# Optimization experiments

Hardware: AMD Instinct MI355X
Metric: run time of the kernel (lower is better)

Reference implementation:

```python
import jax, jax.numpy as jnp
import numpy as np

B, S, D = 1, 4096, 2048
H = 16
HD = D // H  # 128
BASE = 10000.0


def setup_inputs() -> dict:
    key = jax.random.key(0)
    ks = jax.random.split(key, 6)
    hidden_states = jax.random.normal(ks[0], (B, S, D), dtype=jnp.float32)
    position_ids = jnp.broadcast_to(jnp.arange(S, dtype=jnp.int64 if jax.config.jax_enable_x64 else jnp.int32), (B, S))
    scale = 1.0 / np.sqrt(D)
    Wq = jax.random.normal(ks[1], (D, D), dtype=jnp.float32) * scale
    Wk = jax.random.normal(ks[2], (D, D), dtype=jnp.float32) * scale
    Wv = jax.random.normal(ks[3], (D, D), dtype=jnp.float32) * scale
    Wo = jax.random.normal(ks[4], (D, D), dtype=jnp.float32) * scale
    return {"hidden_states": hidden_states, "Wq": Wq, "Wk": Wk, "Wv": Wv, "Wo": Wo, "position_ids": position_ids}


def _rotate_half(x):
    x1, x2 = x[..., : x.shape[-1] // 2], x[..., x.shape[-1] // 2 :]
    return jnp.concatenate((-x2, x1), axis=-1)


def reference(hidden_states, Wq, Wk, Wv, Wo, position_ids):
    # QKV projections (torch Linear: x @ W.T)
    q = hidden_states @ Wq.T  # [B,S,D]
    k = hidden_states @ Wk.T
    v = hidden_states @ Wv.T
    # split heads -> [B,H,S,HD]
    q = q.reshape(B, S, H, HD).transpose(0, 2, 1, 3)
    k = k.reshape(B, S, H, HD).transpose(0, 2, 1, 3)
    v = v.reshape(B, S, H, HD).transpose(0, 2, 1, 3)
    # RoPE tables over seq positions
    inv_freq = 1.0 / (BASE ** (jnp.arange(0, HD, 2, dtype=jnp.float32) / HD))  # [HD/2]
    t = jnp.arange(S, dtype=jnp.float32)
    freqs = t[:, None] * inv_freq[None, :]            # [S, HD/2]
    emb = jnp.concatenate((freqs, freqs), axis=-1)    # [S, HD]
    cos = jnp.cos(emb)[position_ids][:, None]         # [B,1,S,HD]
    sin = jnp.sin(emb)[position_ids][:, None]
    q = q * cos + _rotate_half(q) * sin
    k = k * cos + _rotate_half(k) * sin
    # attention (num_kv_heads == num_heads, so no GQA repeat)
    scores = jnp.einsum("bhqd,bhkd->bhqk", q, k) / jnp.sqrt(jnp.float32(HD))
    attn = jax.nn.softmax(scores, axis=-1)
    out = jnp.einsum("bhqk,bhkd->bhqd", attn, v)      # [B,H,S,HD]
    out = out.transpose(0, 2, 1, 3).reshape(B, S, D)
    return out @ Wo.T
```

## Files before the change

### kernel.cpp

```cpp
#include <hip/hip_runtime.h>
#include <hip/hip_bf16.h>

#define S_LEN 4096
#define DMODEL 2048
#define NHEADS 16
#define HEADDIM 128
#define LDQ 6144

typedef __attribute__((ext_vector_type(8))) short bf16x8;
typedef __attribute__((ext_vector_type(4))) float f32x4;

__device__ __forceinline__ float bf2f(ushort u) {
  union { unsigned int i; float f; } x; x.i = ((unsigned int)u) << 16; return x.f;
}
__device__ __forceinline__ ushort f2bf(float f) {
  union { float f; unsigned int i; } x; x.f = f;
  unsigned int u = x.i;
  unsigned int r = u + 0x7fffu + ((u >> 16) & 1u);
  return (ushort)(r >> 16);
}
__device__ __forceinline__ unsigned int cvtpk(float a, float b) {
  unsigned int r;
  asm("v_cvt_pk_bf16_f32 %0, %1, %2" : "=v"(r) : "v"(a), "v"(b));
  return r;
}
__device__ __forceinline__ float fexp2(float x) {
  float r;
  asm("v_exp_f32 %0, %1" : "=v"(r) : "v"(x));
  return r;
}

__device__ __forceinline__ void gload16(const ushort* g, ushort* l) {
  __builtin_amdgcn_global_load_lds(
      (const __attribute__((address_space(1))) unsigned int*)g,
      (__attribute__((address_space(3))) unsigned int*)l, 16, 0, 0);
}

__global__ __launch_bounds__(256) void rope_table_kernel(float* __restrict__ cosT,
                                                         float* __restrict__ sinT) {
  int idx = blockIdx.x * 256 + threadIdx.x;
  int t = idx >> 6, j = idx & 63;
  float expo = (float)(2 * j) / 128.0f;
  float inv = 1.0f / powf(10000.0f, expo);
  float f = (float)t * inv;
  cosT[idx] = cosf(f);
  sinT[idx] = sinf(f);
}

__global__ __launch_bounds__(256) void convert_kernel(const float* __restrict__ in,
                                                      ushort* __restrict__ hi) {
  int i = (blockIdx.x * 256 + threadIdx.x) * 4;
  float4 v = *reinterpret_cast<const float4*>(&in[i]);
  ushort4 h;
  h.x = f2bf(v.x); h.y = f2bf(v.y); h.z = f2bf(v.z); h.w = f2bf(v.w);
  *reinterpret_cast<ushort4*>(&hi[i]) = h;
}

__global__ __launch_bounds__(256) void prep_weights(const float* __restrict__ Wq,
                                                    const float* __restrict__ Wk,
                                                    const float* __restrict__ Wv,
                                                    const float* __restrict__ Wo,
                                                    ushort* __restrict__ Wqkv,
                                                    ushort* __restrict__ Woh) {
  int i = (blockIdx.x * 256 + threadIdx.x) * 4;
  int which = blockIdx.y;
  const float* src = (which == 0) ? Wq : (which == 1) ? Wk : (which == 2) ? Wv : Wo;
  ushort* dst = (which == 3) ? Woh : (Wqkv + (size_t)which * DMODEL * DMODEL);
  float4 v = *reinterpret_cast<const float4*>(&src[i]);
  ushort4 h;
  h.x = f2bf(v.x); h.y = f2bf(v.y); h.z = f2bf(v.z); h.w = f2bf(v.w);
  *reinterpret_cast<ushort4*>(&dst[i]) = h;
}

__global__ __launch_bounds__(256) void gemm_qkv(const ushort* __restrict__ Ah_,
                                                const ushort* __restrict__ Bh_,
                                                ushort* __restrict__ Cout,
                                                int M, int N, int K) {
  __shared__ __align__(16) ushort sAh[128 * 64], sBh[128 * 64];
  const int tid = threadIdx.x;
  const int wave = tid >> 6, lane = tid & 63;
  const int lg = lane >> 4, lm = lane & 15;
  const int nwg = gridDim.x * gridDim.y;
  const int id = blockIdx.y * gridDim.x + blockIdx.x;
  const int cpx = nwg >> 3;
  const int swz = (id & 7) * cpx + (id >> 3);
  const int nbx = N >> 7;
  const int m0 = (swz / nbx) * 128, n0 = (swz % nbx) * 128;
  const int wm = (wave >> 1) * 64, wn = (wave & 1) * 64;
  f32x4 acc[4][4] = {};

  int srow[4], scc[4], lbs[4];
#pragma unroll
  for (int it = 0; it < 4; ++it) {
    int ci = it * 256 + wave * 64 + lane;
    srow[it] = ci >> 3;
    scc[it] = (ci & 7) ^ (srow[it] & 7);
    lbs[it] = (it * 256 + wave * 64) * 8;
  }

  for (int k0 = 0; k0 < K; k0 += 64) {
    __syncthreads();
#pragma unroll
    for (int it = 0; it < 4; ++it) {
      size_t ga = (size_t)(m0 + srow[it]) * K + k0 + scc[it] * 8;
      size_t gb = (size_t)(n0 + srow[it]) * K + k0 + scc[it] * 8;
      gload16(&Ah_[ga], &sAh[lbs[it]]);
      gload16(&Bh_[gb], &sBh[lbs[it]]);
    }
    __syncthreads();
    bf16x8 ah[4][2], bh[4][2];
#pragma unroll
    for (int t = 0; t < 4; ++t)
#pragma unroll
      for (int kc = 0; kc < 2; ++kc) {
        int Ra = wm + t * 16 + lm;
        int Rb = wn + t * 16 + lm;
        int pa_ = ((kc * 4 + lg) ^ (Ra & 7)) * 8;
        int pb_ = ((kc * 4 + lg) ^ (Rb & 7)) * 8;
        ah[t][kc] = *reinterpret_cast<const bf16x8*>(&sAh[Ra * 64 + pa_]);
        bh[t][kc] = *reinterpret_cast<const bf16x8*>(&sBh[Rb * 64 + pb_]);
      }
#pragma unroll
    for (int kc = 0; kc < 2; ++kc)
#pragma unroll
      for (int mi = 0; mi < 4; ++mi)
#pragma unroll
        for (int ni = 0; ni < 4; ++ni)
          acc[mi][ni] = __builtin_amdgcn_mfma_f32_16x16x32_bf16(ah[mi][kc], bh[ni][kc], acc[mi][ni], 0, 0, 0);
  }
#pragma unroll
  for (int mi = 0; mi < 4; ++mi)
#pragma unroll
    for (int ni = 0; ni < 4; ++ni)
#pragma unroll
      for (int j = 0; j < 4; ++j) {
        int row = m0 + wm + mi * 16 + lg * 4 + j;
        int col = n0 + wn + ni * 16 + lm;
        Cout[(size_t)row * N + col] = f2bf(acc[mi][ni][j]);
      }
}

__global__ __launch_bounds__(256) void gemm1o64(const ushort* __restrict__ Ah_,
                                                const ushort* __restrict__ Bh_,
                                                float* __restrict__ Cout,
                                                int M, int N, int K) {
  __shared__ __align__(16) ushort sAh[128 * 64], sBh[128 * 64];
  const int tid = threadIdx.x;
  const int wave = tid >> 6, lane = tid & 63;
  const int lg = lane >> 4, lm = lane & 15;
  const int nwg = gridDim.x * gridDim.y;
  const int id = blockIdx.y * gridDim.x + blockIdx.x;
  const int cpx = nwg >> 3;
  const int swz = (id & 7) * cpx + (id >> 3);
  const int nbx = N >> 7;
  const int m0 = (swz / nbx) * 128, n0 = (swz % nbx) * 128;
  const int wm = (wave >> 1) * 64, wn = (wave & 1) * 64;
  f32x4 acc[4][4] = {};

  int srow[4], scc[4], lbs[4];
#pragma unroll
  for (int it = 0; it < 4; ++it) {
    int ci = it * 256 + wave * 64 + lane;
    srow[it] = ci >> 3;
    scc[it] = (ci & 7) ^ (srow[it] & 7);
    lbs[it] = (it * 256 + wave * 64) * 8;
  }

  for (int k0 = 0; k0 < K; k0 += 64) {
    __syncthreads();
#pragma unroll
    for (int it = 0; it < 4; ++it) {
      size_t ga = (size_t)(m0 + srow[it]) * K + k0 + scc[it] * 8;
      size_t gb = (size_t)(n0 + srow[it]) * K + k0 + scc[it] * 8;
      gload16(&Ah_[ga], &sAh[lbs[it]]);
      gload16(&Bh_[gb], &sBh[lbs[it]]);
    }
    __syncthreads();
    bf16x8 ah[4][2], bh[4][2];
#pragma unroll
    for (int t = 0; t < 4; ++t)
#pragma unroll
      for (int kc = 0; kc < 2; ++kc) {
        int Ra = wm + t * 16 + lm;
        int Rb = wn + t * 16 + lm;
        int pa_ = ((kc * 4 + lg) ^ (Ra & 7)) * 8;
        int pb_ = ((kc * 4 + lg) ^ (Rb & 7)) * 8;
        ah[t][kc] = *reinterpret_cast<const bf16x8*>(&sAh[Ra * 64 + pa_]);
        bh[t][kc] = *reinterpret_cast<const bf16x8*>(&sBh[Rb * 64 + pb_]);
      }
#pragma unroll
    for (int kc = 0; kc < 2; ++kc)
#pragma unroll
      for (int mi = 0; mi < 4; ++mi)
#pragma unroll
        for (int ni = 0; ni < 4; ++ni)
          acc[mi][ni] = __builtin_amdgcn_mfma_f32_16x16x32_bf16(ah[mi][kc], bh[ni][kc], acc[mi][ni], 0, 0, 0);
  }
#pragma unroll
  for (int mi = 0; mi < 4; ++mi)
#pragma unroll
    for (int ni = 0; ni < 4; ++ni)
#pragma unroll
      for (int j = 0; j < 4; ++j) {
        int row = m0 + wm + mi * 16 + lg * 4 + j;
        int col = n0 + wn + ni * 16 + lm;
        Cout[(size_t)row * N + col] = acc[mi][ni][j];
      }
}

__global__ __launch_bounds__(256) void rope2_kernel(ushort* __restrict__ QKV,
                                                    const int* __restrict__ pos,
                                                    const float* __restrict__ cosT,
                                                    const float* __restrict__ sinT) {
  int t = blockIdx.x * 256 + threadIdx.x;
  int j0 = (t & 7) * 8;
  int hh = (t >> 3) & 15;
  int s = t >> 7;
  int p = pos[s];
  float cs[8], sn[8];
  *reinterpret_cast<float4*>(&cs[0]) = *reinterpret_cast<const float4*>(&cosT[p * 64 + j0]);
  *reinterpret_cast<float4*>(&cs[4]) = *reinterpret_cast<const float4*>(&cosT[p * 64 + j0 + 4]);
  *reinterpret_cast<float4*>(&sn[0]) = *reinterpret_cast<const float4*>(&sinT[p * 64 + j0]);
  *reinterpret_cast<float4*>(&sn[4]) = *reinterpret_cast<const float4*>(&sinT[p * 64 + j0 + 4]);
  size_t base = (size_t)s * LDQ + hh * HEADDIM + j0;
  union u8 { uint4 v; ushort e[8]; };
  u8 qa, qb, ka, kb;
  qa.v = *reinterpret_cast<const uint4*>(&QKV[base]);
  qb.v = *reinterpret_cast<const uint4*>(&QKV[base + 64]);
  ka.v = *reinterpret_cast<const uint4*>(&QKV[base + DMODEL]);
  kb.v = *reinterpret_cast<const uint4*>(&QKV[base + DMODEL + 64]);
  const float scl = 0.12751742f;
#pragma unroll
  for (int e = 0; e < 8; ++e) {
    float q1 = bf2f(qa.e[e]), q2 = bf2f(qb.e[e]);
    float k1 = bf2f(ka.e[e]), k2 = bf2f(kb.e[e]);
    qa.e[e] = f2bf((q1 * cs[e] - q2 * sn[e]) * scl);
    qb.e[e] = f2bf((q2 * cs[e] + q1 * sn[e]) * scl);
    ka.e[e] = f2bf(k1 * cs[e] - k2 * sn[e]);
    kb.e[e] = f2bf(k2 * cs[e] + k1 * sn[e]);
  }
  *reinterpret_cast<uint4*>(&QKV[base]) = qa.v;
  *reinterpret_cast<uint4*>(&QKV[base + 64]) = qb.v;
  *reinterpret_cast<uint4*>(&QKV[base + DMODEL]) = ka.v;
  *reinterpret_cast<uint4*>(&QKV[base + DMODEL + 64]) = kb.v;
}

__global__ __launch_bounds__(256) void transpose_kernel(const ushort* __restrict__ Vr,
                                                        ushort* __restrict__ Vt) {
  __shared__ __align__(16) ushort tile[64 * 72];
  int tid = threadIdx.x;
  int s0 = blockIdx.x * 64, c0 = blockIdx.y * 64;
#pragma unroll
  for (int it = 0; it < 2; ++it) {
    int i = tid + it * 256;
    int r = i >> 3, c = i & 7;
    *reinterpret_cast<uint4*>(&tile[r * 72 + c * 8]) =
        *reinterpret_cast<const uint4*>(&Vr[(size_t)(s0 + r) * LDQ + c0 + c * 8]);
  }
  __syncthreads();
#pragma unroll
  for (int it = 0; it < 2; ++it) {
    int i = tid + it * 256;
    int cr = i >> 3, sc = i & 7;
    ushort tmp[8];
#pragma unroll
    for (int j = 0; j < 8; ++j) tmp[j] = tile[(sc * 8 + j) * 72 + cr];
    *reinterpret_cast<uint4*>(&Vt[(size_t)(c0 + cr) * S_LEN + s0 + sc * 8]) =
        *reinterpret_cast<uint4*>(tmp);
  }
}

__global__ __launch_bounds__(256, 2) void flash12_kernel(const ushort* __restrict__ QKV,
                                                         const ushort* __restrict__ Vt,
                                                         ushort* __restrict__ Oh) {
  __shared__ __align__(16) ushort Kt[2][64 * 128];
  __shared__ __align__(16) ushort Vs[2][128 * 64];
  const int tid = threadIdx.x;
  const int wave = tid >> 6, lane = tid & 63;
  const int lg = lane >> 4, lm = lane & 15;
  const int id = blockIdx.y * gridDim.x + blockIdx.x;
  const int o = (id & 7) * 64 + (id >> 3);
  const int h = o >> 5;
  const int q0 = (o & 31) * 128;

  bf16x8 qh[2][4];
#pragma unroll
  for (int t2 = 0; t2 < 2; ++t2) {
    int qrow = q0 + wave * 32 + t2 * 16 + lm;
#pragma unroll
    for (int kc = 0; kc < 4; ++kc)
      qh[t2][kc] = *reinterpret_cast<const bf16x8*>(
          &QKV[(size_t)qrow * LDQ + h * HEADDIM + kc * 32 + lg * 8]);
  }

  bf16x8 ones;
#pragma unroll
  for (int i = 0; i < 8; ++i) ones[i] = (short)0x3f80;

  auto rho = [](int s) {
    return 32 * ((s >> 4) & 1) + 8 * ((s >> 2) & 3) + 4 * (s >> 5) + (s & 3);
  };
  const ushort* Kb = QKV + DMODEL;
  const ushort* pK[4];
  const ushort* pV[4];
  int lbs[4];
#pragma unroll
  for (int k = 0; k < 4; ++k) {
    int ci = k * 256 + wave * 64 + lane;
    int ks = ci >> 4;
    int kcc = (ci & 15) ^ (ks & 7);
    pK[k] = Kb + (size_t)rho(ks) * LDQ + h * HEADDIM + kcc * 8;
    int vd = ci >> 3;
    int vcc = (ci & 7) ^ (vd & 7);
    pV[k] = Vt + (size_t)(h * HEADDIM + vd) * S_LEN + vcc * 8;
    lbs[k] = (k * 256 + wave * 64) * 8;
  }

  f32x4 oacc[2][8] = {};
  f32x4 osum[2] = {};
  float mrun[2];
#pragma unroll
  for (int t2 = 0; t2 < 2; ++t2) mrun[t2] = -3.0e38f;

#pragma unroll
  for (int k = 0; k < 4; ++k) {
    gload16(pK[k], &Kt[0][lbs[k]]);
    gload16(pV[k], &Vs[0][lbs[k]]);
  }
  __syncthreads();

  for (int t = 0; t < S_LEN / 64; ++t) {
    const int cur = t & 1;
    if (t < S_LEN / 64 - 1) {
      const size_t koff = (size_t)(t + 1) * 64;
#pragma unroll
      for (int k = 0; k < 4; ++k) {
        gload16(pK[k] + koff * LDQ, &Kt[cur ^ 1][lbs[k]]);
        gload16(pV[k] + koff, &Vs[cur ^ 1][lbs[k]]);
      }
    }
    const ushort* Kc = &Kt[cur][0];
    const ushort* Vc = &Vs[cur][0];

    f32x4 st[2][4] = {};
    __builtin_amdgcn_s_setprio(1);
#pragma unroll
    for (int nf = 0; nf < 4; ++nf)
#pragma unroll
      for (int kc = 0; kc < 4; ++kc) {
        int pc = (kc * 4 + lg) ^ (lm & 7);
        bf16x8 kfrag = *reinterpret_cast<const bf16x8*>(&Kc[(nf * 16 + lm) * 128 + pc * 8]);
        st[0][nf] = __builtin_amdgcn_mfma_f32_16x16x32_bf16(kfrag, qh[0][kc], st[0][nf], 0, 0, 0);
        st[1][nf] = __builtin_amdgcn_mfma_f32_16x16x32_bf16(kfrag, qh[1][kc], st[1][nf], 0, 0, 0);
      }
    __builtin_amdgcn_s_setprio(0);

    float m16[2];
#pragma unroll
    for (int t2 = 0; t2 < 2; ++t2) {
      float m = fmaxf(st[t2][0][0], st[t2][0][1]);
      m = fmaxf(fmaxf(m, st[t2][0][2]), st[t2][0][3]);
      m = fmaxf(fmaxf(m, st[t2][1][0]), st[t2][1][1]);
      m = fmaxf(fmaxf(m, st[t2][1][2]), st[t2][1][3]);
      m = fmaxf(fmaxf(m, st[t2][2][0]), st[t2][2][1]);
      m = fmaxf(fmaxf(m, st[t2][2][2]), st[t2][2][3]);
      m = fmaxf(fmaxf(m, st[t2][3][0]), st[t2][3][1]);
      m = fmaxf(fmaxf(m, st[t2][3][2]), st[t2][3][3]);
      m = fmaxf(m, __shfl_xor(m, 16));
      m = fmaxf(m, __shfl_xor(m, 32));
      m16[t2] = m;
    }

    bool grow = (m16[0] > mrun[0] + 11.5f) || (m16[1] > mrun[1] + 11.5f);
    if (__any(grow)) {
#pragma unroll
      for (int t2 = 0; t2 < 2; ++t2) {
        float mn = fmaxf(mrun[t2], m16[t2]);
        float scl = fexp2(mrun[t2] - mn);
        mrun[t2] = mn;
        float sj[4];
#pragma unroll
        for (int j = 0; j < 4; ++j) sj[j] = __shfl(scl, lg * 4 + j);
#pragma unroll
        for (int j = 0; j < 4; ++j) osum[t2][j] *= sj[j];
#pragma unroll
        for (int nb = 0; nb < 8; ++nb)
#pragma unroll
          for (int j = 0; j < 4; ++j) oacc[t2][nb][j] *= sj[j];
      }
    }

#pragma unroll
    for (int t2 = 0; t2 < 2; ++t2)
#pragma unroll
      for (int nf = 0; nf < 4; ++nf)
#pragma unroll
        for (int j = 0; j < 4; ++j)
          st[t2][nf][j] = fexp2(st[t2][nf][j] - mrun[t2]);

    bf16x8 pa[2][2];
#pragma unroll
    for (int t2 = 0; t2 < 2; ++t2)
#pragma unroll
      for (int kk = 0; kk < 2; ++kk) {
        union { unsigned int u[4]; bf16x8 v; } w_;
        w_.u[0] = cvtpk(st[t2][kk][0], st[t2][kk][1]);
        w_.u[1] = cvtpk(st[t2][kk][2], st[t2][kk][3]);
        w_.u[2] = cvtpk(st[t2][2 + kk][0], st[t2][2 + kk][1]);
        w_.u[3] = cvtpk(st[t2][2 + kk][2], st[t2][2 + kk][3]);
        pa[t2][kk] = w_.v;
      }

    __builtin_amdgcn_s_setprio(1);
#pragma unroll
    for (int t2 = 0; t2 < 2; ++t2) {
      osum[t2] = __builtin_amdgcn_mfma_f32_16x16x32_bf16(pa[t2][0], ones, osum[t2], 0, 0, 0);
      osum[t2] = __builtin_amdgcn_mfma_f32_16x16x32_bf16(pa[t2][1], ones, osum[t2], 0, 0, 0);
    }
#pragma unroll
    for (int nb = 0; nb < 8; ++nb)
#pragma unroll
      for (int kk = 0; kk < 2; ++kk) {
        int pc = (kk * 4 + lg) ^ (lm & 7);
        bf16x8 vfrag = *reinterpret_cast<const bf16x8*>(&Vc[(nb * 16 + lm) * 64 + pc * 8]);
        oacc[0][nb] = __builtin_amdgcn_mfma_f32_16x16x32_bf16(pa[0][kk], vfrag, oacc[0][nb], 0, 0, 0);
        oacc[1][nb] = __builtin_amdgcn_mfma_f32_16x16x32_bf16(pa[1][kk], vfrag, oacc[1][nb], 0, 0, 0);
      }
    __builtin_amdgcn_s_setprio(0);

    __syncthreads();
  }

#pragma unroll
  for (int t2 = 0; t2 < 2; ++t2) {
    float linv[4];
#pragma unroll
    for (int j = 0; j < 4; ++j) linv[j] = 1.0f / osum[t2][j];
#pragma unroll
    for (int nb = 0; nb < 8; ++nb)
#pragma unroll
      for (int j = 0; j < 4; ++j) {
        int row = q0 + wave * 32 + t2 * 16 + lg * 4 + j;
        int col = h * HEADDIM + nb * 16 + lm;
        Oh[(size_t)row * DMODEL + col] = f2bf(oacc[t2][nb][j] * linv[j]);
      }
  }
}

extern "C" void kernel_launch(void* const* d_in, const int* in_sizes, int n_in,
                              void* d_out, int out_size, void* d_ws, size_t ws_size,
                              hipStream_t stream) {
  (void)in_sizes; (void)n_in; (void)out_size; (void)ws_size;
  const float* X  = (const float*)d_in[0];
  const float* Wq = (const float*)d_in[1];
  const float* Wk = (const float*)d_in[2];
  const float* Wv = (const float*)d_in[3];
  const float* Wo = (const float*)d_in[4];
  const int* pos  = (const int*)d_in[5];
  float* out = (float*)d_out;

  ushort* wb = (ushort*)d_ws;
  const size_t SD = (size_t)S_LEN * DMODEL;
  const size_t DD = (size_t)DMODEL * DMODEL;

  ushort* Xh   = wb;
  ushort* QKV  = wb + 2 * SD;
  ushort* Vt   = wb + 5 * SD;
  ushort* W0h  = wb + 6 * SD;
  ushort* Wqkv = wb + 7 * SD;
  float* cosT  = (float*)(wb + 9 * SD);
  float* sinT  = cosT + (size_t)S_LEN * 64;
  ushort* OhB  = Wqkv;

  rope_table_kernel<<<S_LEN * 64 / 256, 256, 0, stream>>>(cosT, sinT);
  convert_kernel<<<SD / 1024, 256, 0, stream>>>(X, Xh);
  prep_weights<<<dim3(DD / 1024, 4), 256, 0, stream>>>(Wq, Wk, Wv, Wo, Wqkv, W0h);

  gemm_qkv<<<dim3(LDQ / 128, S_LEN / 128), 256, 0, stream>>>(Xh, Wqkv, QKV, S_LEN, LDQ, DMODEL);

  rope2_kernel<<<(S_LEN * 1024 / 8) / 256, 256, 0, stream>>>(QKV, pos, cosT, sinT);
  transpose_kernel<<<dim3(S_LEN / 64, DMODEL / 64), 256, 0, stream>>>(QKV + 2 * DMODEL, Vt);

  flash12_kernel<<<dim3(32, 16), 256, 0, stream>>>(QKV, Vt, OhB);

  dim3 gemmGrid(DMODEL / 128, S_LEN / 128);
  gemm1o64<<<gemmGrid, 256, 0, stream>>>(OhB, W0h, out, S_LEN, DMODEL, DMODEL);
}
```

Measured before the change: 340.5 us.

## Software-pipeline flash attention by computing next tile's QK^T before the barrier

Restructures the attention main loop into a manually unrolled pair of tile steps with named LDS buffers and two score register sets. After the PV product and the barrier for tile T, the kernel issues the global loads for tile T+2 and immediately computes QK^T for tile T+1. The aim is to let the next tile's score matrix multiplies overlap with the softmax and exponent work instead of serialising them. The cost is a second score accumulator array, which raises register pressure under the 2-blocks-per-CU launch bound and may cause spills.

```diff
diff --git a/kernel.cpp b/kernel.cpp
--- a/kernel.cpp
+++ b/kernel.cpp
@@ -270,11 +270,92 @@
   }
 }
 
-__global__ __launch_bounds__(256, 2) void flash12_kernel(const ushort* __restrict__ QKV,
+#define FTILE(STC, STN, VCUR, KWB, VWB, KRB, T)                                           \
+  {                                                                                       \
+    float m16[2];                                                                         \
+    _Pragma("unroll") for (int t2 = 0; t2 < 2; ++t2) {                                    \
+      float m = fmaxf(STC[t2][0][0], STC[t2][0][1]);                                      \
+      m = fmaxf(fmaxf(m, STC[t2][0][2]), STC[t2][0][3]);                                  \
+      m = fmaxf(fmaxf(m, STC[t2][1][0]), STC[t2][1][1]);                                  \
+      m = fmaxf(fmaxf(m, STC[t2][1][2]), STC[t2][1][3]);                                  \
+      m = fmaxf(fmaxf(m, STC[t2][2][0]), STC[t2][2][1]);                                  \
+      m = fmaxf(fmaxf(m, STC[t2][2][2]), STC[t2][2][3]);                                  \
+      m = fmaxf(fmaxf(m, STC[t2][3][0]), STC[t2][3][1]);                                  \
+      m = fmaxf(fmaxf(m, STC[t2][3][2]), STC[t2][3][3]);                                  \
+      m = fmaxf(m, __shfl_xor(m, 16));                                                    \
+      m = fmaxf(m, __shfl_xor(m, 32));                                                    \
+      m16[t2] = m;                                                                        \
+    }                                                                                     \
+    bool grow = (m16[0] > mrun[0] + 11.5f) || (m16[1] > mrun[1] + 11.5f);                 \
+    if (__any(grow)) {                                                                    \
+      _Pragma("unroll") for (int t2 = 0; t2 < 2; ++t2) {                                  \
+        float mn = fmaxf(mrun[t2], m16[t2]);                                              \
+        float scl = fexp2(mrun[t2] - mn);                                                 \
+        mrun[t2] = mn;                                                                    \
+        float sj[4];                                                                      \
+        _Pragma("unroll") for (int j = 0; j < 4; ++j) sj[j] = __shfl(scl, lg * 4 + j);    \
+        _Pragma("unroll") for (int j = 0; j < 4; ++j) osum[t2][j] *= sj[j];               \
+        _Pragma("unroll") for (int nb = 0; nb < 8; ++nb)                                  \
+            _Pragma("unroll") for (int j = 0; j < 4; ++j) oacc[t2][nb][j] *= sj[j];       \
+      }                                                                                   \
+    }                                                                                     \
+    _Pragma("unroll") for (int t2 = 0; t2 < 2; ++t2)                                      \
+        _Pragma("unroll") for (int nf = 0; nf < 4; ++nf)                                  \
+            _Pragma("unroll") for (int j = 0; j < 4; ++j)                                 \
+                STC[t2][nf][j] = fexp2(STC[t2][nf][j] - mrun[t2]);                        \
+    bf16x8 pa[2][2];                                                                      \
+    _Pragma("unroll") for (int t2 = 0; t2 < 2; ++t2)                                      \
+        _Pragma("unroll") for (int kk = 0; kk < 2; ++kk) {                                \
+      union { unsigned int u[4]; bf16x8 v; } w_;                                          \
+      w_.u[0] = cvtpk(STC[t2][kk][0], STC[t2][kk][1]);                                    \
+      w_.u[1] = cvtpk(STC[t2][kk][2], STC[t2][kk][3]);                                    \
+      w_.u[2] = cvtpk(STC[t2][2 + kk][0], STC[t2][2 + kk][1]);                            \
+      w_.u[3] = cvtpk(STC[t2][2 + kk][2], STC[t2][2 + kk][3]);                            \
+      pa[t2][kk] = w_.v;                                                                  \
+    }                                                                                     \
+    __builtin_amdgcn_s_setprio(1);                                                        \
+    _Pragma("unroll") for (int t2 = 0; t2 < 2; ++t2) {                                    \
+      osum[t2] = __builtin_amdgcn_mfma_f32_16x16x32_bf16(pa[t2][0], ones, osum[t2], 0, 0, 0); \
+      osum[t2] = __builtin_amdgcn_mfma_f32_16x16x32_bf16(pa[t2][1], ones, osum[t2], 0, 0, 0); \
+    }                                                                                     \
+    _Pragma("unroll") for (int nb = 0; nb < 8; ++nb)                                      \
+        _Pragma("unroll") for (int kk = 0; kk < 2; ++kk) {                                \
+      int pc = (kk * 4 + lg) ^ (lm & 7);                                                  \
+      bf16x8 vfrag = *reinterpret_cast<const bf16x8*>(&VCUR[(nb * 16 + lm) * 64 + pc * 8]); \
+      oacc[0][nb] = __builtin_amdgcn_mfma_f32_16x16x32_bf16(pa[0][kk], vfrag, oacc[0][nb], 0, 0, 0); \
+      oacc[1][nb] = __builtin_amdgcn_mfma_f32_16x16x32_bf16(pa[1][kk], vfrag, oacc[1][nb], 0, 0, 0); \
+    }                                                                                     \
+    __builtin_amdgcn_s_setprio(0);                                                        \
+    __syncthreads();                                                                      \
+    if ((T) + 2 < 64) {                                                                   \
+      const size_t ko_ = (size_t)((T) + 2) * 64;                                          \
+      _Pragma("unroll") for (int k = 0; k < 4; ++k) {                                     \
+        gload16(pK[k] + ko_ * LDQ, &KWB[lbs[k]]);                                         \
+        gload16(pV[k] + ko_, &VWB[lbs[k]]);                                               \
+      }                                                                                   \
+    }                                                                                     \
+    if ((T) + 1 < 64) {                                                                   \
+      _Pragma("unroll") for (int t2 = 0; t2 < 2; ++t2)                                    \
+          _Pragma("unroll") for (int nf = 0; nf < 4; ++nf) STN[t2][nf] = fzero;           \
+      __builtin_amdgcn_s_setprio(1);                                                      \
+      _Pragma("unroll") for (int nf = 0; nf < 4; ++nf)                                    \
+          _Pragma("unroll") for (int kc = 0; kc < 4; ++kc) {                              \
+        int pc = (kc * 4 + lg) ^ (lm & 7);                                                \
+        bf16x8 kfrag = *reinterpret_cast<const bf16x8*>(&KRB[(nf * 16 + lm) * 128 + pc * 8]); \
+        STN[0][nf] = __builtin_amdgcn_mfma_f32_16x16x32_bf16(kfrag, qh[0][kc], STN[0][nf], 0, 0, 0); \
+        STN[1][nf] = __builtin_amdgcn_mfma_f32_16x16x32_bf16(kfrag, qh[1][kc], STN[1][nf], 0, 0, 0); \
+      }                                                                                   \
+      __builtin_amdgcn_s_setprio(0);                                                      \
+    }                                                                                     \
+  }
+
+__global__ __launch_bounds__(256, 2) void flash14_kernel(const ushort* __restrict__ QKV,
                                                          const ushort* __restrict__ Vt,
                                                          ushort* __restrict__ Oh) {
-  __shared__ __align__(16) ushort Kt[2][64 * 128];
-  __shared__ __align__(16) ushort Vs[2][128 * 64];
+  __shared__ __align__(16) ushort KtA[64 * 128];
+  __shared__ __align__(16) ushort KtB[64 * 128];
+  __shared__ __align__(16) ushort VsA[128 * 64];
+  __shared__ __align__(16) ushort VsB[128 * 64];
   const int tid = threadIdx.x;
   const int wave = tid >> 6, lane = tid & 63;
   const int lg = lane >> 4, lm = lane & 15;
@@ -282,6 +363,7 @@
   const int o = (id & 7) * 64 + (id >> 3);
   const int h = o >> 5;
   const int q0 = (o & 31) * 128;
+  const f32x4 fzero = {};
 
   bf16x8 qh[2][4];
 #pragma unroll
@@ -324,111 +406,36 @@
 
 #pragma unroll
   for (int k = 0; k < 4; ++k) {
-    gload16(pK[k], &Kt[0][lbs[k]]);
-    gload16(pV[k], &Vs[0][lbs[k]]);
+    gload16(pK[k], &KtA[lbs[k]]);
+    gload16(pV[k], &VsA[lbs[k]]);
   }
   __syncthreads();
-
-  for (int t = 0; t < S_LEN / 64; ++t) {
-    const int cur = t & 1;
-    if (t < S_LEN / 64 - 1) {
-      const size_t koff = (size_t)(t + 1) * 64;
-#pragma unroll
-      for (int k = 0; k < 4; ++k) {
-        gload16(pK[k] + koff * LDQ, &Kt[cur ^ 1][lbs[k]]);
-        gload16(pV[k] + koff, &Vs[cur ^ 1][lbs[k]]);
-      }
+#pragma unroll
+  for (int k = 0; k < 4; ++k) {
+    gload16(pK[k] + (size_t)64 * LDQ, &KtB[lbs[k]]);
+    gload16(pV[k] + 64, &VsB[lbs[k]]);
+  }
+  f32x4 stA[2][4], stB[2][4];
+#pragma unroll
+  for (int t2 = 0; t2 < 2; ++t2)
+#pragma unroll
+    for (int nf = 0; nf < 4; ++nf) stA[t2][nf] = fzero;
+  __builtin_amdgcn_s_setprio(1);
+#pragma unroll
+  for (int nf = 0; nf < 4; ++nf)
+#pragma unroll
+    for (int kc = 0; kc < 4; ++kc) {
+      int pc = (kc * 4 + lg) ^ (lm & 7);
+      bf16x8 kfrag = *reinterpret_cast<const bf16x8*>(&KtA[(nf * 16 + lm) * 128 + pc * 8]);
+      stA[0][nf] = __builtin_amdgcn_mfma_f32_16x16x32_bf16(kfrag, qh[0][kc], stA[0][nf], 0, 0, 0);
+      stA[1][nf] = __builtin_amdgcn_mfma_f32_16x16x32_bf16(kfrag, qh[1][kc], stA[1][nf], 0, 0, 0);
     }
-    const ushort* Kc = &Kt[cur][0];
-    const ushort* Vc = &Vs[cur][0];
-
-    f32x4 st[2][4] = {};
-    __builtin_amdgcn_s_setprio(1);
-#pragma unroll
-    for (int nf = 0; nf < 4; ++nf)
-#pragma unroll
-      for (int kc = 0; kc < 4; ++kc) {
-        int pc = (kc * 4 + lg) ^ (lm & 7);
-        bf16x8 kfrag = *reinterpret_cast<const bf16x8*>(&Kc[(nf * 16 + lm) * 128 + pc * 8]);
-        st[0][nf] = __builtin_amdgcn_mfma_f32_16x16x32_bf16(kfrag, qh[0][kc], st[0][nf], 0, 0, 0);
-        st[1][nf] = __builtin_amdgcn_mfma_f32_16x16x32_bf16(kfrag, qh[1][kc], st[1][nf], 0, 0, 0);
-      }
-    __builtin_amdgcn_s_setprio(0);
-
-    float m16[2];
-#pragma unroll
-    for (int t2 = 0; t2 < 2; ++t2) {
-      float m = fmaxf(st[t2][0][0], st[t2][0][1]);
-      m = fmaxf(fmaxf(m, st[t2][0][2]), st[t2][0][3]);
-      m = fmaxf(fmaxf(m, st[t2][1][0]), st[t2][1][1]);
-      m = fmaxf(fmaxf(m, st[t2][1][2]), st[t2][1][3]);
-      m = fmaxf(fmaxf(m, st[t2][2][0]), st[t2][2][1]);
-      m = fmaxf(fmaxf(m, st[t2][2][2]), st[t2][2][3]);
-      m = fmaxf(fmaxf(m, st[t2][3][0]), st[t2][3][1]);
-      m = fmaxf(fmaxf(m, st[t2][3][2]), st[t2][3][3]);
-      m = fmaxf(m, __shfl_xor(m, 16));
-      m = fmaxf(m, __shfl_xor(m, 32));
-      m16[t2] = m;
-    }
-
-    bool grow = (m16[0] > mrun[0] + 11.5f) || (m16[1] > mrun[1] + 11.5f);
-    if (__any(grow)) {
-#pragma unroll
-      for (int t2 = 0; t2 < 2; ++t2) {
-        float mn = fmaxf(mrun[t2], m16[t2]);
-        float scl = fexp2(mrun[t2] - mn);
-        mrun[t2] = mn;
-        float sj[4];
-#pragma unroll
-        for (int j = 0; j < 4; ++j) sj[j] = __shfl(scl, lg * 4 + j);
-#pragma unroll
-        for (int j = 0; j < 4; ++j) osum[t2][j] *= sj[j];
-#pragma unroll
-        for (int nb = 0; nb < 8; ++nb)
-#pragma unroll
-          for (int j = 0; j < 4; ++j) oacc[t2][nb][j] *= sj[j];
-      }
-    }
-
-#pragma unroll
-    for (int t2 = 0; t2 < 2; ++t2)
-#pragma unroll
-      for (int nf = 0; nf < 4; ++nf)
-#pragma unroll
-        for (int j = 0; j < 4; ++j)
-          st[t2][nf][j] = fexp2(st[t2][nf][j] - mrun[t2]);
-
-    bf16x8 pa[2][2];
-#pragma unroll
-    for (int t2 = 0; t2 < 2; ++t2)
-#pragma unroll
-      for (int kk = 0; kk < 2; ++kk) {
-        union { unsigned int u[4]; bf16x8 v; } w_;
-        w_.u[0] = cvtpk(st[t2][kk][0], st[t2][kk][1]);
-        w_.u[1] = cvtpk(st[t2][kk][2], st[t2][kk][3]);
-        w_.u[2] = cvtpk(st[t2][2 + kk][0], st[t2][2 + kk][1]);
-        w_.u[3] = cvtpk(st[t2][2 + kk][2], st[t2][2 + kk][3]);
-        pa[t2][kk] = w_.v;
-      }
-
-    __builtin_amdgcn_s_setprio(1);
-#pragma unroll
-    for (int t2 = 0; t2 < 2; ++t2) {
-      osum[t2] = __builtin_amdgcn_mfma_f32_16x16x32_bf16(pa[t2][0], ones, osum[t2], 0, 0, 0);
-      osum[t2] = __builtin_amdgcn_mfma_f32_16x16x32_bf16(pa[t2][1], ones, osum[t2], 0, 0, 0);
-    }
-#pragma unroll
-    for (int nb = 0; nb < 8; ++nb)
-#pragma unroll
-      for (int kk = 0; kk < 2; ++kk) {
-        int pc = (kk * 4 + lg) ^ (lm & 7);
-        bf16x8 vfrag = *reinterpret_cast<const bf16x8*>(&Vc[(nb * 16 + lm) * 64 + pc * 8]);
-        oacc[0][nb] = __builtin_amdgcn_mfma_f32_16x16x32_bf16(pa[0][kk], vfrag, oacc[0][nb], 0, 0, 0);
-        oacc[1][nb] = __builtin_amdgcn_mfma_f32_16x16x32_bf16(pa[1][kk], vfrag, oacc[1][nb], 0, 0, 0);
-      }
-    __builtin_amdgcn_s_setprio(0);
-
-    __syncthreads();
+  __builtin_amdgcn_s_setprio(0);
+
+  for (int tp = 0; tp < 32; ++tp) {
+    const int t0 = 2 * tp;
+    FTILE(stA, stB, VsA, KtA, VsA, KtB, t0)
+    FTILE(stB, stA, VsB, KtB, VsB, KtA, t0 + 1)
   }
 
 #pragma unroll
@@ -481,7 +488,7 @@
   rope2_kernel<<<(S_LEN * 1024 / 8) / 256, 256, 0, stream>>>(QKV, pos, cosT, sinT);
   transpose_kernel<<<dim3(S_LEN / 64, DMODEL / 64), 256, 0, stream>>>(QKV + 2 * DMODEL, Vt);
 
-  flash12_kernel<<<dim3(32, 16), 256, 0, stream>>>(QKV, Vt, OhB);
+  flash14_kernel<<<dim3(32, 16), 256, 0, stream>>>(QKV, Vt, OhB);
 
   dim3 gemmGrid(DMODEL / 128, S_LEN / 128);
   gemm1o64<<<gemmGrid, 256, 0, stream>>>(OhB, W0h, out, S_LEN, DMODEL, DMODEL);
```

Measured after the change: 339.9 us. Within noise of the previous version (-0.2%).
